# Kernel tuning notes

Hardware: AMD Instinct MI355X
Metric: run time of the kernel (lower is better)

Reference implementation:

```python
import jax, jax.numpy as jnp
import numpy as np

B, H, S, E = 8, 50, 512, 128
D = 2 * E  # feature dim of inputs


def setup_inputs() -> dict:
    key = jax.random.key(0)
    ks = jax.random.split(key, 10)
    def lin(kw, kb, fan_in, fan_out):
        lim = 1.0 / np.sqrt(fan_in)
        w = jax.random.uniform(kw, (fan_out, fan_in), jnp.float32, -lim, lim)
        b = jax.random.uniform(kb, (fan_out,), jnp.float32, -lim, lim)
        return w, b
    wc_w, wc_b = lin(ks[0], ks[1], D, D)
    wh_w, wh_b = lin(ks[2], ks[3], D, D)
    qt_w, qt_b = lin(ks[4], ks[5], D, 1)
    wf_w, wf_b = lin(ks[6], ks[7], 2 * D, E)
    return {
        "wca_history_embeddings": jax.random.normal(ks[8], (B, H, S, D), jnp.float32),
        "wca_current_embeddings": jax.random.normal(ks[9], (B, S, D), jnp.float32),
        "wc_w": wc_w, "wc_b": wc_b,
        "wh_w": wh_w, "wh_b": wh_b,
        "qt_w": qt_w, "qt_b": qt_b,
        "wf_w": wf_w, "wf_b": wf_b,
    }


def reference(wca_history_embeddings, wca_current_embeddings,
              wc_w, wc_b, wh_w, wh_b, qt_w, qt_b, wf_w, wf_b):
    # history: [B, H, S, D] -> [B, S, H, D]; current: [B, S, D]
    hist = jnp.transpose(wca_history_embeddings, (0, 2, 1, 3))
    wc_out = wca_current_embeddings @ wc_w.T + wc_b          # [B, S, D]
    wh_out = hist @ wh_w.T + wh_b                             # [B, S, H, D]
    combined = jax.nn.sigmoid(wc_out[:, :, None, :] + wh_out) # [B, S, H, D]
    alpha = combined @ qt_w.T + qt_b                          # [B, S, H, 1]
    history_sum = jnp.sum(alpha * hist, axis=2)               # [B, S, D]
    concat = jnp.concatenate([wca_current_embeddings, history_sum], axis=-1)  # [B, S, 2D]
    return concat @ wf_w.T + wf_b                             # [B, S, E]
```

## Files before the change

### kernel.cpp

```cpp
#include <hip/hip_runtime.h>
#include <hip/hip_bf16.h>

#define Hh 50

typedef __attribute__((ext_vector_type(8))) short bf16x8;
typedef __attribute__((ext_vector_type(4))) float f32x4;
typedef __attribute__((ext_vector_type(16))) float f32x16;

static __device__ __forceinline__ short b16(float x) {
    return __builtin_bit_cast(short, __float2bfloat16(x));
}
static __device__ __forceinline__ bf16x8 cvt8(const float* p) {
    f32x4 a = *(const f32x4*)p;
    f32x4 b = *(const f32x4*)(p + 4);
    bf16x8 r;
    r[0] = b16(a[0]); r[1] = b16(a[1]); r[2] = b16(a[2]); r[3] = b16(a[3]);
    r[4] = b16(b[0]); r[5] = b16(b[1]); r[6] = b16(b[2]); r[7] = b16(b[3]);
    return r;
}

__global__ __launch_bounds__(256) void k_prep(const float* __restrict__ w,
                                              short* __restrict__ o) {
    int t = (int)blockIdx.x * 256 + threadIdx.x;
    int nt = t >> 10;
    int ks = (t >> 6) & 15;
    int l  = t & 63;
    int col = nt * 32 + (l & 31);
    int k   = ks * 16 + (l >> 5) * 8;
    bf16x8 v = cvt8(w + (size_t)col * 256 + k);
    *(bf16x8*)(o + (size_t)t * 8) = v;
}

__global__ __launch_bounds__(64) void k_wc(const float* __restrict__ cur,
                                           const float* __restrict__ wcw,
                                           const float* __restrict__ wcb,
                                           float* __restrict__ out) {
    int l = threadIdx.x;
    int m0 = (int)(blockIdx.x >> 2) * 16;
    int ntb = (int)(blockIdx.x & 3) * 4;
    int lk = (l >> 4) * 8;

    bf16x8 Af[8];
#pragma unroll
    for (int k = 0; k < 8; k++)
        Af[k] = cvt8(cur + (size_t)(m0 + (l & 15)) * 256 + k * 32 + lk);

#pragma unroll
    for (int nt = 0; nt < 4; nt++) {
        int col = (ntb + nt) * 16 + (l & 15);
        f32x4 a = {0.f, 0.f, 0.f, 0.f};
#pragma unroll
        for (int k = 0; k < 8; k++) {
            bf16x8 Bf = cvt8(wcw + (size_t)col * 256 + k * 32 + lk);
            a = __builtin_amdgcn_mfma_f32_16x16x32_bf16(Af[k], Bf, a, 0, 0, 0);
        }
        float bias = wcb[col];
        int row = m0 + (l >> 4) * 4;
#pragma unroll
        for (int r = 0; r < 4; r++)
            out[(size_t)(row + r) * 256 + col] = a[r] + bias;
    }
}

__global__ __launch_bounds__(256, 4)
void k_main(const float* __restrict__ hist,
            const float* __restrict__ wc_ws,
            const short* __restrict__ whpk,
            const float* __restrict__ whb,
            const float* __restrict__ qtw,
            const float* __restrict__ qtb,
            float* __restrict__ hsum_ws) {
    __shared__ __align__(16) char histA[64 * 512];
    __shared__ float wcrow[256];
    __shared__ float qtl[256];
    __shared__ float alphaP[4][32];
    __shared__ float alphaF[64];

    int tid = threadIdx.x;
    int l = tid & 63;
    int w = tid >> 6;
    int b = (int)(blockIdx.x >> 9);
    int s = (int)(blockIdx.x & 511);

    for (int c = tid; c < 1600; c += 256) {
        int r = c >> 5, g = c & 31;
        bf16x8 v = cvt8(hist + ((size_t)(b * Hh + r) * 512 + s) * 256 + g * 8);
        *(bf16x8*)(&histA[r * 512 + ((g ^ (r & 15)) << 4)]) = v;
    }
    if (tid < 448) {
        int r = 50 + (tid >> 5), g = tid & 31;
        *(f32x4*)(&histA[r * 512 + ((g ^ (r & 15)) << 4)]) = (f32x4){0.f, 0.f, 0.f, 0.f};
    }
    wcrow[tid] = wc_ws[(size_t)(b * 512 + s) * 256 + tid] + whb[tid];
    qtl[tid] = qtw[tid];
    __syncthreads();

    int p = w & 1, nh = w >> 1;

    bf16x8 Af[16];
    {
        int r = p * 32 + (l & 31);
#pragma unroll
        for (int ks = 0; ks < 16; ks++) {
            int g = ks * 2 + (l >> 5);
            Af[ks] = *(const bf16x8*)(&histA[r * 512 + ((g ^ (r & 15)) << 4)]);
        }
    }

    float pal[16];
#pragma unroll
    for (int i = 0; i < 16; i++) pal[i] = 0.f;

    const short* wq = whpk + (size_t)l * 8;
#pragma unroll 1
    for (int nt = nh * 4; nt < nh * 4 + 4; nt++) {
        f32x16 acc;
#pragma unroll
        for (int i = 0; i < 16; i++) acc[i] = 0.f;
        bf16x8 bc = *(const bf16x8*)(wq + (size_t)(nt * 16) * 512);
#pragma unroll
        for (int ks = 0; ks < 16; ks++) {
            bf16x8 bn;
            if (ks < 15) bn = *(const bf16x8*)(wq + (size_t)(nt * 16 + ks + 1) * 512);
            acc = __builtin_amdgcn_mfma_f32_32x32x16_bf16(Af[ks], bc, acc, 0, 0, 0);
            bc = bn;
        }
        int col = nt * 32 + (l & 31);
        float qv = qtl[col], wb = wcrow[col];
#pragma unroll
        for (int r = 0; r < 16; r++) {
            float v = acc[r] + wb;
            float sg = __builtin_amdgcn_rcpf(1.0f + __expf(-v));
            pal[r] += qv * sg;
        }
    }

#pragma unroll
    for (int r = 0; r < 16; r++) {
        float v = pal[r];
        v += __shfl_xor(v, 1);
        v += __shfl_xor(v, 2);
        v += __shfl_xor(v, 4);
        v += __shfl_xor(v, 8);
        v += __shfl_xor(v, 16);
        if ((l & 31) == 0) {
            int rowIn = (r & 3) + 8 * (r >> 2) + 4 * (l >> 5);
            alphaP[w][rowIn] = v;
        }
    }
    __syncthreads();
    if (tid < Hh) {
        int pp = tid >> 5, ri = tid & 31;
        alphaF[tid] = qtb[0] + alphaP[pp][ri] + alphaP[2 + pp][ri];
    }
    __syncthreads();

    {
        int d = tid;
        float a = 0.f;
#pragma unroll 2
        for (int h = 0; h < Hh; h++) {
            int g = (d >> 3) ^ (h & 15);
            unsigned short u = *(const unsigned short*)(&histA[h * 512 + (g << 4) + (d & 7) * 2]);
            unsigned int x = ((unsigned int)u) << 16;
            a += alphaF[h] * __builtin_bit_cast(float, x);
        }
        hsum_ws[(size_t)(b * 512 + s) * 256 + d] = a;
    }
}

__global__ __launch_bounds__(64) void k_wf(const float* __restrict__ cur,
                                           const float* __restrict__ hsum,
                                           const float* __restrict__ wfw,
                                           const float* __restrict__ wfb,
                                           float* __restrict__ out) {
    int l = threadIdx.x;
    int m0 = (int)(blockIdx.x >> 1) * 16;
    int ntb = (int)(blockIdx.x & 1) * 4;
    int lk = (l >> 4) * 8;

    f32x4 acc[4];
#pragma unroll
    for (int nt = 0; nt < 4; nt++) acc[nt] = (f32x4){0.f, 0.f, 0.f, 0.f};

#pragma unroll
    for (int k = 0; k < 16; k++) {
        int row = m0 + (l & 15);
        bf16x8 Af;
        if (k < 8)
            Af = cvt8(cur + (size_t)row * 256 + k * 32 + lk);
        else
            Af = cvt8(hsum + (size_t)row * 256 + (k - 8) * 32 + lk);
#pragma unroll
        for (int nt = 0; nt < 4; nt++) {
            int col = (ntb + nt) * 16 + (l & 15);
            bf16x8 Bf = cvt8(wfw + (size_t)col * 512 + k * 32 + lk);
            acc[nt] = __builtin_amdgcn_mfma_f32_16x16x32_bf16(Af, Bf, acc[nt], 0, 0, 0);
        }
    }
#pragma unroll
    for (int nt = 0; nt < 4; nt++) {
        int col = (ntb + nt) * 16 + (l & 15);
        float bias = wfb[col];
        int row = m0 + (l >> 4) * 4;
#pragma unroll
        for (int r = 0; r < 4; r++)
            out[(size_t)(row + r) * 128 + col] = acc[nt][r] + bias;
    }
}

extern "C" void kernel_launch(void* const* d_in, const int* in_sizes, int n_in,
                              void* d_out, int out_size, void* d_ws, size_t ws_size,
                              hipStream_t stream) {
    const float* hist = (const float*)d_in[0];
    const float* cur  = (const float*)d_in[1];
    const float* wc_w = (const float*)d_in[2];
    const float* wc_b = (const float*)d_in[3];
    const float* wh_w = (const float*)d_in[4];
    const float* wh_b = (const float*)d_in[5];
    const float* qt_w = (const float*)d_in[6];
    const float* qt_b = (const float*)d_in[7];
    const float* wf_w = (const float*)d_in[8];
    const float* wf_b = (const float*)d_in[9];

    float* wc_ws = (float*)d_ws;
    float* hsum  = (float*)((char*)d_ws + ((size_t)4 << 20));
    short* whpk  = (short*)((char*)d_ws + ((size_t)8 << 20));

    k_prep<<<32, 256, 0, stream>>>(wh_w, whpk);
    k_wc<<<1024, 64, 0, stream>>>(cur, wc_w, wc_b, wc_ws);
    k_main<<<4096, 256, 0, stream>>>(hist, wc_ws, whpk, wh_b, qt_w, qt_b, hsum);
    k_wf<<<512, 64, 0, stream>>>(cur, hsum, wf_w, wf_b, (float*)d_out);
}
```

Before: 135.4 us.

## Split attention into per-(batch,history) alpha kernel and separate weighted-sum kernel

```diff
diff --git a/kernel.cpp b/kernel.cpp
--- a/kernel.cpp
+++ b/kernel.cpp
@@ -22,10 +22,10 @@
 __global__ __launch_bounds__(256) void k_prep(const float* __restrict__ w,
                                               short* __restrict__ o) {
     int t = (int)blockIdx.x * 256 + threadIdx.x;
-    int nt = t >> 10;
+    int p  = t >> 10;
     int ks = (t >> 6) & 15;
     int l  = t & 63;
-    int col = nt * 32 + (l & 31);
+    int col = p * 32 + (l & 31);
     int k   = ks * 16 + (l >> 5) * 8;
     bf16x8 v = cvt8(w + (size_t)col * 256 + k);
     *(bf16x8*)(o + (size_t)t * 8) = v;
@@ -34,6 +34,7 @@
 __global__ __launch_bounds__(64) void k_wc(const float* __restrict__ cur,
                                            const float* __restrict__ wcw,
                                            const float* __restrict__ wcb,
+                                           const float* __restrict__ whb,
                                            float* __restrict__ out) {
     int l = threadIdx.x;
     int m0 = (int)(blockIdx.x >> 2) * 16;
@@ -54,7 +55,7 @@
             bf16x8 Bf = cvt8(wcw + (size_t)col * 256 + k * 32 + lk);
             a = __builtin_amdgcn_mfma_f32_16x16x32_bf16(Af[k], Bf, a, 0, 0, 0);
         }
-        float bias = wcb[col];
+        float bias = wcb[col] + whb[col];
         int row = m0 + (l >> 4) * 4;
 #pragma unroll
         for (int r = 0; r < 4; r++)
@@ -63,110 +64,107 @@
 }
 
 __global__ __launch_bounds__(256, 4)
-void k_main(const float* __restrict__ hist,
-            const float* __restrict__ wc_ws,
-            const short* __restrict__ whpk,
-            const float* __restrict__ whb,
-            const float* __restrict__ qtw,
-            const float* __restrict__ qtb,
-            float* __restrict__ hsum_ws) {
+void k_alpha(const float* __restrict__ hist,
+             const float* __restrict__ wcplus,
+             const short* __restrict__ whpk,
+             const float* __restrict__ qtw,
+             const float* __restrict__ qtb,
+             float* __restrict__ alphaWS) {
     __shared__ __align__(16) char histA[64 * 512];
-    __shared__ float wcrow[256];
-    __shared__ float qtl[256];
-    __shared__ float alphaP[4][32];
-    __shared__ float alphaF[64];
+    __shared__ float alphaP[8][64];
 
     int tid = threadIdx.x;
     int l = tid & 63;
     int w = tid >> 6;
-    int b = (int)(blockIdx.x >> 9);
-    int s = (int)(blockIdx.x & 511);
-
-    for (int c = tid; c < 1600; c += 256) {
+    int x = (int)blockIdx.x;
+    int b = x / 400;
+    int rem = x - b * 400;
+    int h = rem >> 3;
+    int s0 = (rem & 7) * 64;
+
+    const float* hsrc = hist + ((size_t)(b * Hh + h) * 512 + s0) * 256;
+#pragma unroll
+    for (int i = 0; i < 8; i++) {
+        int c = tid + i * 256;
         int r = c >> 5, g = c & 31;
-        bf16x8 v = cvt8(hist + ((size_t)(b * Hh + r) * 512 + s) * 256 + g * 8);
+        bf16x8 v = cvt8(hsrc + r * 256 + g * 8);
         *(bf16x8*)(&histA[r * 512 + ((g ^ (r & 15)) << 4)]) = v;
     }
-    if (tid < 448) {
-        int r = 50 + (tid >> 5), g = tid & 31;
-        *(f32x4*)(&histA[r * 512 + ((g ^ (r & 15)) << 4)]) = (f32x4){0.f, 0.f, 0.f, 0.f};
-    }
-    wcrow[tid] = wc_ws[(size_t)(b * 512 + s) * 256 + tid] + whb[tid];
-    qtl[tid] = qtw[tid];
     __syncthreads();
 
-    int p = w & 1, nh = w >> 1;
-
-    bf16x8 Af[16];
-    {
-        int r = p * 32 + (l & 31);
-#pragma unroll
-        for (int ks = 0; ks < 16; ks++) {
-            int g = ks * 2 + (l >> 5);
-            Af[ks] = *(const bf16x8*)(&histA[r * 512 + ((g ^ (r & 15)) << 4)]);
+#pragma unroll 1
+    for (int pi = 0; pi < 2; pi++) {
+        int p = w + pi * 4;
+        const short* wqp = whpk + ((size_t)(p * 16) * 64 + l) * 8;
+        bf16x8 Af[16];
+#pragma unroll
+        for (int ks = 0; ks < 16; ks++)
+            Af[ks] = *(const bf16x8*)(wqp + ks * 512);
+
+#pragma unroll 1
+        for (int nt = 0; nt < 2; nt++) {
+            int sl = nt * 32 + (l & 31);
+            int s = s0 + sl;
+
+            f32x16 acc;
+#pragma unroll
+            for (int i = 0; i < 16; i++) acc[i] = 0.f;
+#pragma unroll
+            for (int ks = 0; ks < 16; ks++) {
+                int g = ks * 2 + (l >> 5);
+                bf16x8 Bf = *(const bf16x8*)(&histA[sl * 512 + ((g ^ (sl & 15)) << 4)]);
+                acc = __builtin_amdgcn_mfma_f32_32x32x16_bf16(Af[ks], Bf, acc, 0, 0, 0);
+            }
+
+            const float* wbp = wcplus + (size_t)(b * 512 + s) * 256 + p * 32 + 4 * (l >> 5);
+            const float* qp = qtw + p * 32 + 4 * (l >> 5);
+            float pal = 0.f;
+#pragma unroll
+            for (int q = 0; q < 4; q++) {
+                f32x4 wq = *(const f32x4*)(wbp + 8 * q);
+                f32x4 qv = *(const f32x4*)(qp + 8 * q);
+#pragma unroll
+                for (int j = 0; j < 4; j++) {
+                    float v = acc[q * 4 + j] + wq[j];
+                    float sg = __builtin_amdgcn_rcpf(1.0f + __expf(-v));
+                    pal += qv[j] * sg;
+                }
+            }
+            pal += __shfl_xor(pal, 32);
+            if (l < 32) alphaP[p][sl] = pal;
         }
     }
-
-    float pal[16];
-#pragma unroll
-    for (int i = 0; i < 16; i++) pal[i] = 0.f;
-
-    const short* wq = whpk + (size_t)l * 8;
-#pragma unroll 1
-    for (int nt = nh * 4; nt < nh * 4 + 4; nt++) {
-        f32x16 acc;
-#pragma unroll
-        for (int i = 0; i < 16; i++) acc[i] = 0.f;
-        bf16x8 bc = *(const bf16x8*)(wq + (size_t)(nt * 16) * 512);
-#pragma unroll
-        for (int ks = 0; ks < 16; ks++) {
-            bf16x8 bn;
-            if (ks < 15) bn = *(const bf16x8*)(wq + (size_t)(nt * 16 + ks + 1) * 512);
-            acc = __builtin_amdgcn_mfma_f32_32x32x16_bf16(Af[ks], bc, acc, 0, 0, 0);
-            bc = bn;
-        }
-        int col = nt * 32 + (l & 31);
-        float qv = qtl[col], wb = wcrow[col];
-#pragma unroll
-        for (int r = 0; r < 16; r++) {
-            float v = acc[r] + wb;
-            float sg = __builtin_amdgcn_rcpf(1.0f + __expf(-v));
-            pal[r] += qv * sg;
-        }
-    }
-
-#pragma unroll
-    for (int r = 0; r < 16; r++) {
-        float v = pal[r];
-        v += __shfl_xor(v, 1);
-        v += __shfl_xor(v, 2);
-        v += __shfl_xor(v, 4);
-        v += __shfl_xor(v, 8);
-        v += __shfl_xor(v, 16);
-        if ((l & 31) == 0) {
-            int rowIn = (r & 3) + 8 * (r >> 2) + 4 * (l >> 5);
-            alphaP[w][rowIn] = v;
-        }
-    }
     __syncthreads();
-    if (tid < Hh) {
-        int pp = tid >> 5, ri = tid & 31;
-        alphaF[tid] = qtb[0] + alphaP[pp][ri] + alphaP[2 + pp][ri];
-    }
-    __syncthreads();
-
-    {
-        int d = tid;
-        float a = 0.f;
+
+    if (tid < 64) {
+        float a = qtb[0];
+#pragma unroll
+        for (int p = 0; p < 8; p++) a += alphaP[p][tid];
+        alphaWS[(size_t)(b * Hh + h) * 512 + s0 + tid] = a;
+    }
+}
+
+__global__ __launch_bounds__(256, 8)
+void k_hsum(const float* __restrict__ hist,
+            const float* __restrict__ alphaWS,
+            float* __restrict__ hsum) {
+    int tid = threadIdx.x;
+    int x = (int)blockIdx.x;
+    int b = x >> 7, sc = x & 127;
+    int s = sc * 4 + (tid >> 6);
+    int d = (tid & 63) * 4;
+
+    const float* hp = hist + ((size_t)(b * Hh) * 512 + s) * 256 + d;
+    const float* ap = alphaWS + (size_t)(b * Hh) * 512 + s;
+    f32x4 acc = {0.f, 0.f, 0.f, 0.f};
 #pragma unroll 2
-        for (int h = 0; h < Hh; h++) {
-            int g = (d >> 3) ^ (h & 15);
-            unsigned short u = *(const unsigned short*)(&histA[h * 512 + (g << 4) + (d & 7) * 2]);
-            unsigned int x = ((unsigned int)u) << 16;
-            a += alphaF[h] * __builtin_bit_cast(float, x);
-        }
-        hsum_ws[(size_t)(b * 512 + s) * 256 + d] = a;
-    }
+    for (int h = 0; h < Hh; h++) {
+        f32x4 v = *(const f32x4*)(hp + (size_t)h * 512 * 256);
+        float a = ap[(size_t)h * 512];
+        acc[0] += a * v[0]; acc[1] += a * v[1];
+        acc[2] += a * v[2]; acc[3] += a * v[3];
+    }
+    *(f32x4*)(hsum + ((size_t)b * 512 + s) * 256 + d) = acc;
 }
 
 __global__ __launch_bounds__(64) void k_wf(const float* __restrict__ cur,
@@ -223,12 +221,14 @@
     const float* wf_w = (const float*)d_in[8];
     const float* wf_b = (const float*)d_in[9];
 
-    float* wc_ws = (float*)d_ws;
-    float* hsum  = (float*)((char*)d_ws + ((size_t)4 << 20));
-    short* whpk  = (short*)((char*)d_ws + ((size_t)8 << 20));
+    float* wc_ws   = (float*)d_ws;
+    float* hsum    = (float*)((char*)d_ws + ((size_t)4 << 20));
+    short* whpk    = (short*)((char*)d_ws + ((size_t)8 << 20));
+    float* alphaWS = (float*)((char*)d_ws + ((size_t)8 << 20) + 131072);
 
     k_prep<<<32, 256, 0, stream>>>(wh_w, whpk);
-    k_wc<<<1024, 64, 0, stream>>>(cur, wc_w, wc_b, wc_ws);
-    k_main<<<4096, 256, 0, stream>>>(hist, wc_ws, whpk, wh_b, qt_w, qt_b, hsum);
+    k_wc<<<1024, 64, 0, stream>>>(cur, wc_w, wc_b, wh_b, wc_ws);
+    k_alpha<<<3200, 256, 0, stream>>>(hist, wc_ws, whpk, qt_w, qt_b, alphaWS);
+    k_hsum<<<1024, 256, 0, stream>>>(hist, alphaWS, hsum);
     k_wf<<<512, 64, 0, stream>>>(cur, hsum, wf_w, wf_b, (float*)d_out);
 }
```

Result: slower. 147.5 us (+8.9%).

## Retile main GEMM to 16x16x32 MFMA with per-wave 64-column slices

Applied to the files above, without the earlier changes.

```diff
diff --git a/kernel.cpp b/kernel.cpp
--- a/kernel.cpp
+++ b/kernel.cpp
@@ -5,7 +5,6 @@
 
 typedef __attribute__((ext_vector_type(8))) short bf16x8;
 typedef __attribute__((ext_vector_type(4))) float f32x4;
-typedef __attribute__((ext_vector_type(16))) float f32x16;
 
 static __device__ __forceinline__ short b16(float x) {
     return __builtin_bit_cast(short, __float2bfloat16(x));
@@ -22,11 +21,11 @@
 __global__ __launch_bounds__(256) void k_prep(const float* __restrict__ w,
                                               short* __restrict__ o) {
     int t = (int)blockIdx.x * 256 + threadIdx.x;
-    int nt = t >> 10;
-    int ks = (t >> 6) & 15;
+    int p  = t >> 9;
+    int ks = (t >> 6) & 7;
     int l  = t & 63;
-    int col = nt * 32 + (l & 31);
-    int k   = ks * 16 + (l >> 5) * 8;
+    int col = p * 16 + (l & 15);
+    int k   = ks * 32 + (l >> 4) * 8;
     bf16x8 v = cvt8(w + (size_t)col * 256 + k);
     *(bf16x8*)(o + (size_t)t * 8) = v;
 }
@@ -73,7 +72,7 @@
     __shared__ __align__(16) char histA[64 * 512];
     __shared__ float wcrow[256];
     __shared__ float qtl[256];
-    __shared__ float alphaP[4][32];
+    __shared__ float alphaP[4][64];
     __shared__ float alphaF[64];
 
     int tid = threadIdx.x;
@@ -95,64 +94,83 @@
     qtl[tid] = qtw[tid];
     __syncthreads();
 
-    int p = w & 1, nh = w >> 1;
-
-    bf16x8 Af[16];
-    {
-        int r = p * 32 + (l & 31);
-#pragma unroll
-        for (int ks = 0; ks < 16; ks++) {
-            int g = ks * 2 + (l >> 5);
-            Af[ks] = *(const bf16x8*)(&histA[r * 512 + ((g ^ (r & 15)) << 4)]);
-        }
-    }
-
-    float pal[16];
-#pragma unroll
-    for (int i = 0; i < 16; i++) pal[i] = 0.f;
-
-    const short* wq = whpk + (size_t)l * 8;
-#pragma unroll 1
-    for (int nt = nh * 4; nt < nh * 4 + 4; nt++) {
-        f32x16 acc;
-#pragma unroll
-        for (int i = 0; i < 16; i++) acc[i] = 0.f;
-        bf16x8 bc = *(const bf16x8*)(wq + (size_t)(nt * 16) * 512);
-#pragma unroll
-        for (int ks = 0; ks < 16; ks++) {
-            bf16x8 bn;
-            if (ks < 15) bn = *(const bf16x8*)(wq + (size_t)(nt * 16 + ks + 1) * 512);
-            acc = __builtin_amdgcn_mfma_f32_32x32x16_bf16(Af[ks], bc, acc, 0, 0, 0);
-            bc = bn;
-        }
-        int col = nt * 32 + (l & 31);
-        float qv = qtl[col], wb = wcrow[col];
-#pragma unroll
-        for (int r = 0; r < 16; r++) {
-            float v = acc[r] + wb;
-            float sg = __builtin_amdgcn_rcpf(1.0f + __expf(-v));
-            pal[r] += qv * sg;
-        }
-    }
-
-#pragma unroll
-    for (int r = 0; r < 16; r++) {
-        float v = pal[r];
-        v += __shfl_xor(v, 1);
-        v += __shfl_xor(v, 2);
-        v += __shfl_xor(v, 4);
-        v += __shfl_xor(v, 8);
-        v += __shfl_xor(v, 16);
-        if ((l & 31) == 0) {
-            int rowIn = (r & 3) + 8 * (r >> 2) + 4 * (l >> 5);
-            alphaP[w][rowIn] = v;
+    bf16x8 Ab[2][4], Bb[2][4];
+    auto LDA = [&](bf16x8(&A)[4], int ks) {
+#pragma unroll
+        for (int m = 0; m < 4; m++) {
+            int rA = m * 16 + (l & 15);
+            int g = ks * 4 + (l >> 4);
+            A[m] = *(const bf16x8*)(&histA[rA * 512 + ((g ^ (rA & 15)) << 4)]);
+        }
+    };
+    auto LDB = [&](bf16x8(&Bf)[4], int ks) {
+#pragma unroll
+        for (int nt = 0; nt < 4; nt++) {
+            int p = w * 4 + nt;
+            Bf[nt] = *(const bf16x8*)(whpk + ((size_t)((p * 8 + ks) * 64 + l)) * 8);
+        }
+    };
+
+    f32x4 acc[4][4];
+#pragma unroll
+    for (int m = 0; m < 4; m++)
+#pragma unroll
+        for (int nt = 0; nt < 4; nt++)
+            acc[m][nt] = (f32x4){0.f, 0.f, 0.f, 0.f};
+
+    LDA(Ab[0], 0);
+    LDB(Bb[0], 0);
+#pragma unroll
+    for (int ks = 0; ks < 8; ks++) {
+        int cur = ks & 1, nxt = cur ^ 1;
+        if (ks < 7) {
+            LDA(Ab[nxt], ks + 1);
+            LDB(Bb[nxt], ks + 1);
+        }
+#pragma unroll
+        for (int m = 0; m < 4; m++)
+#pragma unroll
+            for (int nt = 0; nt < 4; nt++)
+                acc[m][nt] = __builtin_amdgcn_mfma_f32_16x16x32_bf16(
+                    Ab[cur][m], Bb[cur][nt], acc[m][nt], 0, 0, 0);
+    }
+
+    float pal[4][4];
+#pragma unroll
+    for (int m = 0; m < 4; m++)
+#pragma unroll
+        for (int r = 0; r < 4; r++) pal[m][r] = 0.f;
+
+#pragma unroll
+    for (int m = 0; m < 4; m++) {
+#pragma unroll
+        for (int nt = 0; nt < 4; nt++) {
+            int col = w * 64 + nt * 16 + (l & 15);
+            float qv = qtl[col], wb = wcrow[col];
+#pragma unroll
+            for (int r = 0; r < 4; r++) {
+                float v = acc[m][nt][r] + wb;
+                pal[m][r] += qv * __builtin_amdgcn_rcpf(1.0f + __expf(-v));
+            }
+        }
+    }
+
+#pragma unroll
+    for (int m = 0; m < 4; m++) {
+#pragma unroll
+        for (int r = 0; r < 4; r++) {
+            float v = pal[m][r];
+            v += __shfl_xor(v, 1);
+            v += __shfl_xor(v, 2);
+            v += __shfl_xor(v, 4);
+            v += __shfl_xor(v, 8);
+            if ((l & 15) == 0)
+                alphaP[w][m * 16 + (l >> 4) * 4 + r] = v;
         }
     }
     __syncthreads();
-    if (tid < Hh) {
-        int pp = tid >> 5, ri = tid & 31;
-        alphaF[tid] = qtb[0] + alphaP[pp][ri] + alphaP[2 + pp][ri];
-    }
+    if (tid < Hh)
+        alphaF[tid] = qtb[0] + alphaP[0][tid] + alphaP[1][tid] + alphaP[2][tid] + alphaP[3][tid];
     __syncthreads();
 
     {
```

New measurement: 129.4 us. 4.4% less time.
